# Optimization experiments

Hardware: AMD Instinct MI355X
Metric: run time of the kernel (lower is better)

Reference implementation:

```python
import jax, jax.numpy as jnp
import numpy as np

NORM_EPS = 1e-12  # torch F.normalize default eps (module's self.eps is unused)


def setup_inputs() -> dict:
    key = jax.random.key(0)
    k1, k2 = jax.random.split(key)
    src_feat = jax.random.normal(k1, (4, 2048, 128), dtype=jnp.float32)
    tgt_feat = jax.random.normal(k2, (4, 2048, 128), dtype=jnp.float32)
    return {"src_feat": src_feat, "tgt_feat": tgt_feat}


def reference(src_feat, tgt_feat):
    # src_feat: [B,N,C], tgt_feat: [B,M,C]
    # Cosine similarity via normalized matmul instead of [B,N,M,C] broadcast.
    src_sq = jnp.sum(src_feat * src_feat, axis=-1)          # [B,N]
    tgt_sq = jnp.sum(tgt_feat * tgt_feat, axis=-1)          # [B,M]
    src_n = src_feat / jnp.maximum(jnp.sqrt(src_sq), NORM_EPS)[..., None]
    tgt_n = tgt_feat / jnp.maximum(jnp.sqrt(tgt_sq), NORM_EPS)[..., None]
    cosine_sim = jnp.einsum('bnc,bmc->bnm', src_n, tgt_n)   # [B,N,M]
    # Squared L2 distance via ||s||^2 + ||t||^2 - 2 s.t (clamped for numerics)
    dots = jnp.einsum('bnc,bmc->bnm', src_feat, tgt_feat)   # [B,N,M]
    dist_sq = src_sq[:, :, None] + tgt_sq[:, None, :] - 2.0 * dots
    feat_dist = jnp.sqrt(jnp.maximum(dist_sq, 0.0))
    feat_dist_normalized = 1.0 / (1.0 + feat_dist)
    # [B,N,M,2]
    return jnp.stack([cosine_sim, feat_dist_normalized], axis=-1)
```

## Files before the change

kernel.cpp:

```cpp
#include <hip/hip_runtime.h>

#define BATCH 4
#define NDIM 2048
#define MDIM 2048
#define CDIM 128

typedef short bf16x8 __attribute__((ext_vector_type(8)));
typedef float f32x4  __attribute__((ext_vector_type(4)));

__device__ __forceinline__ unsigned short f2bf(float f) {
    union { float f; unsigned int u; } v; v.f = f;
    unsigned int u = v.u;
    return (unsigned short)((u + 0x7FFFu + ((u >> 16) & 1u)) >> 16);
}

__global__ __launch_bounds__(256) void norm_kernel(
    const float* __restrict__ src, const float* __restrict__ tgt,
    float* __restrict__ ws)
{
    int gid  = blockIdx.x * 256 + threadIdx.x;
    int wid  = gid >> 6;
    int lane = gid & 63;
    const float* base = (wid < BATCH * NDIM)
        ? (src + (size_t)wid * CDIM)
        : (tgt + (size_t)(wid - BATCH * NDIM) * CDIM);
    float2 v = ((const float2*)base)[lane];
    float s = v.x * v.x + v.y * v.y;
    #pragma unroll
    for (int off = 32; off >= 1; off >>= 1) s += __shfl_xor(s, off, 64);
    if (lane == 0) ws[wid] = s;
}

__global__ __launch_bounds__(256) void sim_mfma(
    const float* __restrict__ src, const float* __restrict__ tgt,
    const float* __restrict__ ws, float* __restrict__ out)
{
    __shared__ unsigned short As[128 * 128];
    __shared__ unsigned short Bs[128 * 128];

    const int tid = threadIdx.x;
    const int b   = blockIdx.z;
    const int i0  = blockIdx.y << 7;
    const int j0  = blockIdx.x << 7;

    const float4* s4 = (const float4*)(src + ((size_t)b * NDIM + i0) * CDIM);
    const float4* t4 = (const float4*)(tgt + ((size_t)b * MDIM + j0) * CDIM);

    #pragma unroll 4
    for (int it = 0; it < 16; ++it) {
        int idx  = tid + it * 256;
        int row  = idx >> 5;
        int c4   = idx & 31;
        float4 va = s4[idx];
        float4 vb = t4[idx];
        int chunk = c4 >> 1;
        int half  = c4 & 1;
        int off   = row * 128 + (((chunk ^ (row & 15)) << 3) + (half << 2));
        ushort4 ua, ub;
        ua.x = f2bf(va.x); ua.y = f2bf(va.y); ua.z = f2bf(va.z); ua.w = f2bf(va.w);
        ub.x = f2bf(vb.x); ub.y = f2bf(vb.y); ub.z = f2bf(vb.z); ub.w = f2bf(vb.w);
        *(ushort4*)&As[off] = ua;
        *(ushort4*)&Bs[off] = ub;
    }
    __syncthreads();

    const int wave = tid >> 6;
    const int lane = tid & 63;
    const int wm   = (wave & 1) << 6;
    const int wn   = (wave >> 1) << 6;
    const int l16  = lane & 15;
    const int q    = lane >> 4;

    f32x4 acc[4][4];
    #pragma unroll
    for (int i = 0; i < 4; ++i)
        #pragma unroll
        for (int j = 0; j < 4; ++j) acc[i][j] = (f32x4){0.f, 0.f, 0.f, 0.f};

    #pragma unroll
    for (int k0 = 0; k0 < 4; ++k0) {
        int chunk = (k0 << 2) + q;
        int swz   = (chunk ^ l16) << 3;
        bf16x8 a[4], bv[4];
        #pragma unroll
        for (int i = 0; i < 4; ++i)
            a[i] = *(const bf16x8*)&As[(wm + (i << 4) + l16) * 128 + swz];
        #pragma unroll
        for (int j = 0; j < 4; ++j)
            bv[j] = *(const bf16x8*)&Bs[(wn + (j << 4) + l16) * 128 + swz];
        #pragma unroll
        for (int i = 0; i < 4; ++i)
            #pragma unroll
            for (int j = 0; j < 4; ++j)
                acc[i][j] = __builtin_amdgcn_mfma_f32_16x16x32_bf16(
                    a[i], bv[j], acc[i][j], 0, 0, 0);
    }

    const float* nrmS = ws + (size_t)b * NDIM + i0;
    const float* nrmT = ws + (size_t)BATCH * NDIM + (size_t)b * MDIM + j0;

    float sq[4][4], isq[4][4];
    #pragma unroll
    for (int i = 0; i < 4; ++i) {
        float4 s4v = *(const float4*)&nrmS[wm + (i << 4) + (q << 2)];
        sq[i][0] = s4v.x; sq[i][1] = s4v.y; sq[i][2] = s4v.z; sq[i][3] = s4v.w;
        #pragma unroll
        for (int r = 0; r < 4; ++r)
            isq[i][r] = __builtin_amdgcn_rsqf(fmaxf(sq[i][r], 1e-24f));
    }
    float tq[4], itq[4];
    #pragma unroll
    for (int j = 0; j < 4; ++j) {
        tq[j]  = nrmT[wn + (j << 4) + l16];
        itq[j] = __builtin_amdgcn_rsqf(fmaxf(tq[j], 1e-24f));
    }

    float2* out2 = (float2*)out;
    #pragma unroll
    for (int i = 0; i < 4; ++i) {
        #pragma unroll
        for (int r = 0; r < 4; ++r) {
            int mrow = wm + (i << 4) + (q << 2) + r;
            size_t rowbase = ((size_t)b * NDIM + (size_t)(i0 + mrow)) * MDIM + j0;
            float sqr = sq[i][r], isr = isq[i][r];
            #pragma unroll
            for (int j = 0; j < 4; ++j) {
                int ncol = wn + (j << 4) + l16;
                float d   = acc[i][j][r];
                float cs  = d * isr * itq[j];
                float dsq = sqr + tq[j] - 2.0f * d;
                float fd  = __builtin_amdgcn_sqrtf(fmaxf(dsq, 0.0f));
                float fdn = __builtin_amdgcn_rcpf(1.0f + fd);
                out2[rowbase + ncol] = make_float2(cs, fdn);
            }
        }
    }
}

extern "C" void kernel_launch(void* const* d_in, const int* in_sizes, int n_in,
                              void* d_out, int out_size, void* d_ws, size_t ws_size,
                              hipStream_t stream) {
    const float* src = (const float*)d_in[0];
    const float* tgt = (const float*)d_in[1];
    float* ws  = (float*)d_ws;
    float* out = (float*)d_out;

    norm_kernel<<<dim3(4096), dim3(256), 0, stream>>>(src, tgt, ws);

    dim3 grid(MDIM / 128, NDIM / 128, BATCH);
    sim_mfma<<<grid, dim3(256), 0, stream>>>(src, tgt, ws, out);
}
```

Baseline: 147.6 us.

## Pre-convert inputs to swizzled bf16 in prep kernel and DMA tiles to LDS

The norm kernel now also writes a pre-swizzled bf16 copy of src and tgt into the workspace. The main kernel loads its tiles straight into LDS with global_load_lds, so each block no longer re-reads fp32 data and converts it. This halves the global read traffic per tile and drops the per-block conversion ALU work, at the cost of an extra 4 MB write in the prep kernel. Output stores are also made nontemporal, and the distance expression uses an fma.

```diff
diff --git a/kernel.cpp b/kernel.cpp
--- a/kernel.cpp
+++ b/kernel.cpp
@@ -7,14 +7,19 @@
 
 typedef short bf16x8 __attribute__((ext_vector_type(8)));
 typedef float f32x4  __attribute__((ext_vector_type(4)));
+typedef float f32x2  __attribute__((ext_vector_type(2)));
 
-__device__ __forceinline__ unsigned short f2bf(float f) {
-    union { float f; unsigned int u; } v; v.f = f;
-    unsigned int u = v.u;
-    return (unsigned short)((u + 0x7FFFu + ((u >> 16) & 1u)) >> 16);
+#define WS_BF16_OFF 16384
+
+__device__ __forceinline__ unsigned int pack2bf(float lo, float hi) {
+    union { float f; unsigned int u; } a, b;
+    a.f = lo; b.f = hi;
+    unsigned int ua = (a.u + 0x7FFFu + ((a.u >> 16) & 1u)) >> 16;
+    unsigned int ub = (b.u + 0x7FFFu + ((b.u >> 16) & 1u)) & 0xFFFF0000u;
+    return ua | ub;
 }
 
-__global__ __launch_bounds__(256) void norm_kernel(
+__global__ __launch_bounds__(256) void prep_kernel(
     const float* __restrict__ src, const float* __restrict__ tgt,
     float* __restrict__ ws)
 {
@@ -25,6 +30,12 @@
         ? (src + (size_t)wid * CDIM)
         : (tgt + (size_t)(wid - BATCH * NDIM) * CDIM);
     float2 v = ((const float2*)base)[lane];
+
+    unsigned short* wsbf = (unsigned short*)(ws + WS_BF16_OFF);
+    int pos = ((lane >> 2) ^ (wid & 15));
+    *(unsigned int*)&wsbf[(size_t)wid * 128 + pos * 8 + (lane & 3) * 2] =
+        pack2bf(v.x, v.y);
+
     float s = v.x * v.x + v.y * v.y;
     #pragma unroll
     for (int off = 32; off >= 1; off >>= 1) s += __shfl_xor(s, off, 64);
@@ -32,7 +43,6 @@
 }
 
 __global__ __launch_bounds__(256) void sim_mfma(
-    const float* __restrict__ src, const float* __restrict__ tgt,
     const float* __restrict__ ws, float* __restrict__ out)
 {
     __shared__ unsigned short As[128 * 128];
@@ -43,33 +53,32 @@
     const int i0  = blockIdx.y << 7;
     const int j0  = blockIdx.x << 7;
 
-    const float4* s4 = (const float4*)(src + ((size_t)b * NDIM + i0) * CDIM);
-    const float4* t4 = (const float4*)(tgt + ((size_t)b * MDIM + j0) * CDIM);
+    const unsigned short* wsbf = (const unsigned short*)(ws + WS_BF16_OFF);
+    const unsigned short* gA = wsbf + ((size_t)b * NDIM + i0) * 128;
+    const unsigned short* gB = wsbf + ((size_t)(BATCH * NDIM) + (size_t)b * MDIM + j0) * 128;
 
-    #pragma unroll 4
-    for (int it = 0; it < 16; ++it) {
-        int idx  = tid + it * 256;
-        int row  = idx >> 5;
-        int c4   = idx & 31;
-        float4 va = s4[idx];
-        float4 vb = t4[idx];
-        int chunk = c4 >> 1;
-        int half  = c4 & 1;
-        int off   = row * 128 + (((chunk ^ (row & 15)) << 3) + (half << 2));
-        ushort4 ua, ub;
-        ua.x = f2bf(va.x); ua.y = f2bf(va.y); ua.z = f2bf(va.z); ua.w = f2bf(va.w);
-        ub.x = f2bf(vb.x); ub.y = f2bf(vb.y); ub.z = f2bf(vb.z); ub.w = f2bf(vb.w);
-        *(ushort4*)&As[off] = ua;
-        *(ushort4*)&Bs[off] = ub;
+    const int wave = tid >> 6;
+    const int lane = tid & 63;
+
+    {
+        int slot0 = wave * 512;
+        #pragma unroll
+        for (int k = 0; k < 8; ++k) {
+            int s = slot0 + k * 64;
+            __builtin_amdgcn_global_load_lds(
+                (const __attribute__((address_space(1))) void*)(gA + (size_t)(s + lane) * 8),
+                (__attribute__((address_space(3))) void*)&As[s * 8], 16, 0, 0);
+            __builtin_amdgcn_global_load_lds(
+                (const __attribute__((address_space(1))) void*)(gB + (size_t)(s + lane) * 8),
+                (__attribute__((address_space(3))) void*)&Bs[s * 8], 16, 0, 0);
+        }
     }
     __syncthreads();
 
-    const int wave = tid >> 6;
-    const int lane = tid & 63;
-    const int wm   = (wave & 1) << 6;
-    const int wn   = (wave >> 1) << 6;
-    const int l16  = lane & 15;
-    const int q    = lane >> 4;
+    const int wm  = (wave & 1) << 6;
+    const int wn  = (wave >> 1) << 6;
+    const int l16 = lane & 15;
+    const int q   = lane >> 4;
 
     f32x4 acc[4][4];
     #pragma unroll
@@ -115,7 +124,7 @@
         itq[j] = __builtin_amdgcn_rsqf(fmaxf(tq[j], 1e-24f));
     }
 
-    float2* out2 = (float2*)out;
+    f32x2* out2 = (f32x2*)out;
     #pragma unroll
     for (int i = 0; i < 4; ++i) {
         #pragma unroll
@@ -128,10 +137,11 @@
                 int ncol = wn + (j << 4) + l16;
                 float d   = acc[i][j][r];
                 float cs  = d * isr * itq[j];
-                float dsq = sqr + tq[j] - 2.0f * d;
+                float dsq = fmaf(-2.0f, d, sqr + tq[j]);
                 float fd  = __builtin_amdgcn_sqrtf(fmaxf(dsq, 0.0f));
                 float fdn = __builtin_amdgcn_rcpf(1.0f + fd);
-                out2[rowbase + ncol] = make_float2(cs, fdn);
+                f32x2 val = {cs, fdn};
+                __builtin_nontemporal_store(val, &out2[rowbase + ncol]);
             }
         }
     }
@@ -145,8 +155,8 @@
     float* ws  = (float*)d_ws;
     float* out = (float*)d_out;
 
-    norm_kernel<<<dim3(4096), dim3(256), 0, stream>>>(src, tgt, ws);
+    prep_kernel<<<dim3(4096), dim3(256), 0, stream>>>(src, tgt, ws);
 
     dim3 grid(MDIM / 128, NDIM / 128, BATCH);
-    sim_mfma<<<grid, dim3(256), 0, stream>>>(src, tgt, ws, out);
+    sim_mfma<<<grid, dim3(256), 0, stream>>>(ws, out);
 }
```

After: 151.1 us. 2.4% more time.
